# Performance work log

Measured on AMD Instinct MI355X. Metric: run time of the kernel, lower is better.

Reference implementation:

```python
import jax, jax.numpy as jnp
import numpy as np
from jax import lax
import math

B, C_IN, C_OUT, D, H, W = 8, 32, 32, 16, 64, 64
K = 3            # kernel_size (cubic)
PAD = 1
E = 8            # num_experts
GROUPS = 1


def setup_inputs() -> dict:
    key = jax.random.key(0)
    k1, k2, k3, k4 = jax.random.split(key, 4)
    x = jax.random.normal(k1, (B, C_IN, D, H, W), dtype=jnp.float32)
    routing_weights = jax.random.uniform(k2, (B, E), dtype=jnp.float32)
    # kaiming_uniform_(a=sqrt(5)) equivalent bounds
    fan_in = (C_IN // GROUPS) * K * K * K
    gain = math.sqrt(2.0 / (1.0 + 5.0))
    w_bound = gain * math.sqrt(3.0 / fan_in)
    weight = jax.random.uniform(k3, (E, C_OUT, C_IN // GROUPS, K, K, K),
                                dtype=jnp.float32, minval=-w_bound, maxval=w_bound)
    b_bound = 1.0 / math.sqrt(fan_in)
    bias = jax.random.uniform(k4, (E, C_OUT), dtype=jnp.float32,
                              minval=-b_bound, maxval=b_bound)
    return {"x": x, "routing_weights": routing_weights, "weight": weight, "bias": bias}


def reference(x, routing_weights, weight, bias):
    # Faithful to the original einsum: 'bi,eocdwh->bocdwh' sums i and e
    # independently (outer-sum semantics), exactly as torch.einsum does.
    eff_kernel = jnp.einsum('bi,eocdwh->bocdwh', routing_weights, weight)  # [B,O,I/g,kd,kh,kw]
    eff_bias = jnp.einsum('bi,eo->bo', routing_weights, bias)              # [B,O]

    def conv_one(xi, ki, bi):
        # xi: [C_in,D,H,W]; ki: [O, I/g, kd,kh,kw]
        y = lax.conv_general_dilated(
            xi[None], ki,
            window_strides=(1, 1, 1),
            padding=[(PAD, PAD)] * 3,
            lhs_dilation=(1, 1, 1),
            rhs_dilation=(1, 1, 1),
            dimension_numbers=('NCDHW', 'OIDHW', 'NCDHW'),
            feature_group_count=GROUPS,
        )[0]
        return y + bi[:, None, None, None]

    return jax.vmap(conv_one)(x, eff_kernel, eff_bias)  # [B, C_OUT, D, H, W]
```

## Files before the change

kernel.cpp:

```cpp
#include <hip/hip_runtime.h>
#include <hip/hip_bf16.h>

typedef short short8 __attribute__((ext_vector_type(8)));
typedef float f32x4 __attribute__((ext_vector_type(4)));

#define WF_OFF  0u
#define RWB_OFF 55296u
#define RWS_OFF 56320u

__device__ __forceinline__ unsigned bf16rne(float f) {
    unsigned u = __float_as_uint(f);
    return (u + 0x7FFFu + ((u >> 16) & 1u)) >> 16;
}

__global__ void condconv_prep(const float* __restrict__ rw,
                              const float* __restrict__ weight,
                              const float* __restrict__ bias,
                              char* __restrict__ ws) {
    int i = blockIdx.x * 256 + threadIdx.x;
    if (i < 27648) {
        int t   = i >> 10;
        int rem = i & 1023;
        int ot  = rem >> 9;
        int l   = (rem >> 3) & 63;
        int j   = rem & 7;
        int o   = ot * 16 + (l & 15);
        int c   = 8 * (l >> 4) + j;
        float s = 0.f;
#pragma unroll
        for (int e = 0; e < 8; ++e) s += weight[((e * 32 + o) * 32 + c) * 27 + t];
        ((unsigned short*)(ws + WF_OFF))[i] = (unsigned short)bf16rne(s);
    } else if (i < 27904) {
        int k = i - 27648;
        int b = k >> 5, o = k & 31;
        float rs = 0.f, bs = 0.f;
#pragma unroll
        for (int e = 0; e < 8; ++e) { rs += rw[b * 8 + e]; bs += bias[e * 32 + o]; }
        ((float*)(ws + RWB_OFF))[k] = rs * bs;
        if (o == 0) ((float*)(ws + RWS_OFF))[b] = rs;
    }
}

__global__ __launch_bounds__(256, 2) void condconv_fused(
        const float* __restrict__ x,
        const char* __restrict__ wf,
        const float* __restrict__ rwbias,
        const float* __restrict__ rwsum,
        float* __restrict__ out) {
    __shared__ uint4 smem4[4752];
    char* smem = (char*)smem4;

    const int tid  = threadIdx.x;
    const int wv   = tid >> 6;
    const int lane = tid & 63;
    const int n    = lane & 15;
    const int quad = lane >> 4;
    const int y0   = blockIdx.x * 4;
    const int z    = blockIdx.y;
    const int b    = blockIdx.z;
    const int xn   = wv * 16 + n;

    if (tid < 144) {
        int row = tid >> 3, rem = tid & 7;
        int side = rem >> 2, q = rem & 3;
        *(uint4*)(smem + (row * 66 + side * 65) * 64 + q * 16) = make_uint4(0, 0, 0, 0);
    }

    const float* xb = x + (size_t)b * (32 * 16 * 64 * 64);
#pragma unroll
    for (int i = 0; i < 9; ++i) {
        const int s   = tid + i * 256;
        const int row = s >> 7;
        const int rem = s & 127;
        const int c4  = rem & 7;
        const int x4  = rem >> 3;
        const int zp  = row / 6, yp = row - zp * 6;
        const int gz  = z + zp - 1, gy = y0 + yp - 1;
        float4 v0 = {0, 0, 0, 0}, v1 = v0, v2 = v0, v3 = v0;
        if ((unsigned)gz < 16u && (unsigned)gy < 64u) {
            const float* p = xb + (((size_t)(4 * c4) * 16 + gz) * 64 + gy) * 64 + 4 * x4;
            v0 = *(const float4*)(p);
            v1 = *(const float4*)(p + 65536);
            v2 = *(const float4*)(p + 131072);
            v3 = *(const float4*)(p + 196608);
        }
        const float a0[4] = {v0.x, v0.y, v0.z, v0.w};
        const float a1[4] = {v1.x, v1.y, v1.z, v1.w};
        const float a2[4] = {v2.x, v2.y, v2.z, v2.w};
        const float a3[4] = {v3.x, v3.y, v3.z, v3.w};
#pragma unroll
        for (int xi = 0; xi < 4; ++xi) {
            union { __hip_bfloat162 h2[2]; uint2 u; } g;
            g.h2[0] = __float22bfloat162_rn(make_float2(a0[xi], a1[xi]));
            g.h2[1] = __float22bfloat162_rn(make_float2(a2[xi], a3[xi]));
            *(uint2*)(smem + (row * 66 + 4 * x4 + xi + 1) * 64 + c4 * 8) = g.u;
        }
    }
    __syncthreads();

    f32x4 acc[2][4] = {};
    const char* wb = wf + lane * 16;

#pragma unroll
    for (int dz = 0; dz < 3; ++dz) {
        short8 wreg[9][2];
#pragma unroll
        for (int tt = 0; tt < 9; ++tt) {
            wreg[tt][0] = *(const short8*)(wb + ((dz * 9 + tt) * 2 + 0) * 1024);
            wreg[tt][1] = *(const short8*)(wb + ((dz * 9 + tt) * 2 + 1) * 1024);
        }
#pragma unroll
        for (int yq = 0; yq < 6; ++yq) {
#pragma unroll
            for (int dx = 0; dx < 3; ++dx) {
                short8 xf = *(const short8*)(
                    smem + ((dz * 6 + yq) * 66 + xn + dx) * 64 + quad * 16);
#pragma unroll
                for (int dy = 0; dy < 3; ++dy) {
                    const int r = yq - dy;
                    if (r >= 0 && r < 4) {
                        acc[0][r] = __builtin_amdgcn_mfma_f32_16x16x32_bf16(
                            wreg[dy * 3 + dx][0], xf, acc[0][r], 0, 0, 0);
                        acc[1][r] = __builtin_amdgcn_mfma_f32_16x16x32_bf16(
                            wreg[dy * 3 + dx][1], xf, acc[1][r], 0, 0, 0);
                    }
                }
            }
        }
    }

    const float rwb = rwsum[b];
#pragma unroll
    for (int ot = 0; ot < 2; ++ot)
#pragma unroll
        for (int reg = 0; reg < 4; ++reg) {
            const int o = ot * 16 + quad * 4 + reg;
            const float bb = rwbias[b * 32 + o];
            const size_t obase = ((size_t)(b * 32 + o) * 16 + z) * 64;
#pragma unroll
            for (int r = 0; r < 4; ++r)
                out[(obase + y0 + r) * 64 + xn] = rwb * acc[ot][r][reg] + bb;
        }
}

extern "C" void kernel_launch(void* const* d_in, const int* in_sizes, int n_in,
                              void* d_out, int out_size, void* d_ws, size_t ws_size,
                              hipStream_t stream) {
    const float* x      = (const float*)d_in[0];
    const float* rw     = (const float*)d_in[1];
    const float* weight = (const float*)d_in[2];
    const float* bias   = (const float*)d_in[3];
    float* out = (float*)d_out;
    char*  ws  = (char*)d_ws;

    condconv_prep<<<109, 256, 0, stream>>>(rw, weight, bias, ws);
    condconv_fused<<<dim3(16, 16, 8), 256, 0, stream>>>(
        x, ws + WF_OFF,
        (const float*)(ws + RWB_OFF), (const float*)(ws + RWS_OFF), out);
}
```

Measured before the change: 167.0 us.

## Stage input one depth plane at a time with swizzled padded LDS layout

The kernel used to load all three input depth planes into shared memory before computing. It now loads and converts one z-plane per dz step and computes on it, which cuts the LDS footprint to about a third and raises the launch bound from 2 to 3 blocks per CU. The LDS rows get a padded 72-byte pixel stride and an XOR swizzle on the channel chunk to reduce bank conflicts, so the MFMA operand is now read as two 8-byte loads. Planes outside the depth range skip both the load and the MFMA work. In exchange there are extra block barriers, and global loads are serialized against compute inside each block, which relies on the higher occupancy to hide latency.

```diff
diff --git a/kernel.cpp b/kernel.cpp
--- a/kernel.cpp
+++ b/kernel.cpp
@@ -2,11 +2,16 @@
 #include <hip/hip_bf16.h>
 
 typedef short short8 __attribute__((ext_vector_type(8)));
+typedef short short4v __attribute__((ext_vector_type(4)));
 typedef float f32x4 __attribute__((ext_vector_type(4)));
 
 #define WF_OFF  0u
 #define RWB_OFF 55296u
 #define RWS_OFF 56320u
+
+#define XS 72
+#define RS (66 * XS)
+#define PLANE (6 * RS)
 
 __device__ __forceinline__ unsigned bf16rne(float f) {
     unsigned u = __float_as_uint(f);
@@ -41,14 +46,13 @@
     }
 }
 
-__global__ __launch_bounds__(256, 2) void condconv_fused(
+__global__ __launch_bounds__(256, 3) void condconv_fused(
         const float* __restrict__ x,
         const char* __restrict__ wf,
         const float* __restrict__ rwbias,
         const float* __restrict__ rwsum,
         float* __restrict__ out) {
-    __shared__ uint4 smem4[4752];
-    char* smem = (char*)smem4;
+    __shared__ __align__(16) char smem[PLANE];
 
     const int tid  = threadIdx.x;
     const int wv   = tid >> 6;
@@ -60,69 +64,76 @@
     const int b    = blockIdx.z;
     const int xn   = wv * 16 + n;
 
-    if (tid < 144) {
-        int row = tid >> 3, rem = tid & 7;
-        int side = rem >> 2, q = rem & 3;
-        *(uint4*)(smem + (row * 66 + side * 65) * 64 + q * 16) = make_uint4(0, 0, 0, 0);
+    if (tid < 48) {
+        int yp = tid >> 3, side = (tid >> 2) & 1, q = tid & 3;
+        *(uint4*)(smem + yp * RS + side * 65 * XS + q * 16) = make_uint4(0, 0, 0, 0);
     }
 
-    const float* xb = x + (size_t)b * (32 * 16 * 64 * 64);
-#pragma unroll
-    for (int i = 0; i < 9; ++i) {
-        const int s   = tid + i * 256;
-        const int row = s >> 7;
-        const int rem = s & 127;
-        const int c4  = rem & 7;
-        const int x4  = rem >> 3;
-        const int zp  = row / 6, yp = row - zp * 6;
-        const int gz  = z + zp - 1, gy = y0 + yp - 1;
-        float4 v0 = {0, 0, 0, 0}, v1 = v0, v2 = v0, v3 = v0;
-        if ((unsigned)gz < 16u && (unsigned)gy < 64u) {
-            const float* p = xb + (((size_t)(4 * c4) * 16 + gz) * 64 + gy) * 64 + 4 * x4;
-            v0 = *(const float4*)(p);
-            v1 = *(const float4*)(p + 65536);
-            v2 = *(const float4*)(p + 131072);
-            v3 = *(const float4*)(p + 196608);
-        }
-        const float a0[4] = {v0.x, v0.y, v0.z, v0.w};
-        const float a1[4] = {v1.x, v1.y, v1.z, v1.w};
-        const float a2[4] = {v2.x, v2.y, v2.z, v2.w};
-        const float a3[4] = {v3.x, v3.y, v3.z, v3.w};
-#pragma unroll
-        for (int xi = 0; xi < 4; ++xi) {
-            union { __hip_bfloat162 h2[2]; uint2 u; } g;
-            g.h2[0] = __float22bfloat162_rn(make_float2(a0[xi], a1[xi]));
-            g.h2[1] = __float22bfloat162_rn(make_float2(a2[xi], a3[xi]));
-            *(uint2*)(smem + (row * 66 + 4 * x4 + xi + 1) * 64 + c4 * 8) = g.u;
-        }
-    }
-    __syncthreads();
-
     f32x4 acc[2][4] = {};
-    const char* wb = wf + lane * 16;
+    const float* xb = x + (size_t)b * 2097152;
+    const char* wbase = wf + lane * 16;
 
 #pragma unroll
     for (int dz = 0; dz < 3; ++dz) {
-        short8 wreg[9][2];
+        const int gz = z + dz - 1;
+        const bool gzok = (unsigned)gz < 16u;
+
+        __syncthreads();
+        if (gzok) {
 #pragma unroll
-        for (int tt = 0; tt < 9; ++tt) {
-            wreg[tt][0] = *(const short8*)(wb + ((dz * 9 + tt) * 2 + 0) * 1024);
-            wreg[tt][1] = *(const short8*)(wb + ((dz * 9 + tt) * 2 + 1) * 1024);
+            for (int it = 0; it < 3; ++it) {
+                const int s  = it * 256 + tid;
+                const int x4 = s & 15;
+                const int c4 = (s >> 4) & 7;
+                const int yp = s >> 7;
+                const int gy = y0 + yp - 1;
+                float4 v0 = {0, 0, 0, 0}, v1 = v0, v2 = v0, v3 = v0;
+                if ((unsigned)gy < 64u) {
+                    const float* p = xb + (size_t)c4 * 262144 + gz * 4096 + gy * 64 + 4 * x4;
+                    v0 = *(const float4*)(p);
+                    v1 = *(const float4*)(p + 65536);
+                    v2 = *(const float4*)(p + 131072);
+                    v3 = *(const float4*)(p + 196608);
+                }
+                const float a0[4] = {v0.x, v0.y, v0.z, v0.w};
+                const float a1[4] = {v1.x, v1.y, v1.z, v1.w};
+                const float a2[4] = {v2.x, v2.y, v2.z, v2.w};
+                const float a3[4] = {v3.x, v3.y, v3.z, v3.w};
+#pragma unroll
+                for (int xi = 0; xi < 4; ++xi) {
+                    union { __hip_bfloat162 h2[2]; uint2 u; } g;
+                    g.h2[0] = __float22bfloat162_rn(make_float2(a0[xi], a1[xi]));
+                    g.h2[1] = __float22bfloat162_rn(make_float2(a2[xi], a3[xi]));
+                    const int X = 4 * x4 + xi + 1;
+                    *(uint2*)(smem + yp * RS + X * XS + ((c4 ^ ((X & 3) << 1)) << 3)) = g.u;
+                }
+            }
         }
+        __syncthreads();
+
+        if (gzok) {
+            short8 wreg[18];
+            const char* wp = wbase + dz * 18432;
 #pragma unroll
-        for (int yq = 0; yq < 6; ++yq) {
+            for (int t = 0; t < 18; ++t) wreg[t] = *(const short8*)(wp + t * 1024);
 #pragma unroll
-            for (int dx = 0; dx < 3; ++dx) {
-                short8 xf = *(const short8*)(
-                    smem + ((dz * 6 + yq) * 66 + xn + dx) * 64 + quad * 16);
+            for (int yq = 0; yq < 6; ++yq) {
 #pragma unroll
-                for (int dy = 0; dy < 3; ++dy) {
-                    const int r = yq - dy;
-                    if (r >= 0 && r < 4) {
-                        acc[0][r] = __builtin_amdgcn_mfma_f32_16x16x32_bf16(
-                            wreg[dy * 3 + dx][0], xf, acc[0][r], 0, 0, 0);
-                        acc[1][r] = __builtin_amdgcn_mfma_f32_16x16x32_bf16(
-                            wreg[dy * 3 + dx][1], xf, acc[1][r], 0, 0, 0);
+                for (int dx = 0; dx < 3; ++dx) {
+                    const int X = xn + dx;
+                    const char* rp = smem + yq * RS + X * XS + ((quad ^ (X & 3)) << 4);
+                    union { short8 v; short4v h[2]; } xf;
+                    xf.h[0] = *(const short4v*)rp;
+                    xf.h[1] = *(const short4v*)(rp + 8);
+#pragma unroll
+                    for (int dy = 0; dy < 3; ++dy) {
+                        const int r = yq - dy;
+                        if (r >= 0 && r < 4) {
+                            acc[0][r] = __builtin_amdgcn_mfma_f32_16x16x32_bf16(
+                                wreg[(dy * 3 + dx) * 2 + 0], xf.v, acc[0][r], 0, 0, 0);
+                            acc[1][r] = __builtin_amdgcn_mfma_f32_16x16x32_bf16(
+                                wreg[(dy * 3 + dx) * 2 + 1], xf.v, acc[1][r], 0, 0, 0);
+                        }
                     }
                 }
             }
```

New measurement: 152.6 us. 8.6% less time.
